# Optimization experiments

Measured on AMD Instinct MI355X. Metric: run time of the kernel, lower is better.

Reference implementation:

```python
import jax, jax.numpy as jnp
import numpy as np

B, LQ, LK = 4, 2048, 2048
DQ, DK, DO = 1024, 1024, 1024


def setup_inputs() -> dict:
    key = jax.random.key(0)
    ks = jax.random.split(key, 9)
    s = 0.02
    return {
        "query_input": jax.random.normal(ks[0], (B, LQ, DQ), jnp.float32),
        "key_input": jax.random.normal(ks[1], (B, LK, DK), jnp.float32),
        "value_input": jax.random.normal(ks[2], (B, LK, DK), jnp.float32),
        "Wq": jax.random.normal(ks[3], (DQ, DO), jnp.float32) * s,
        "bq": jax.random.normal(ks[4], (DO,), jnp.float32) * s,
        "Wk": jax.random.normal(ks[5], (DK, DO), jnp.float32) * s,
        "bk": jax.random.normal(ks[6], (DO,), jnp.float32) * s,
        "Wv": jax.random.normal(ks[7], (DK, DO), jnp.float32) * s,
        "bv": jax.random.normal(ks[8], (DO,), jnp.float32) * s,
    }


def reference(query_input, key_input, value_input, Wq, bq, Wk, bk, Wv, bv):
    scale = jnp.asarray(DO, query_input.dtype) ** 0.5
    q = query_input @ Wq + bq              # [B, Lq, D]
    k = key_input @ Wk + bk                # [B, Lk, D]
    v = value_input @ Wv + bv              # [B, Lk, D]
    attn = jnp.einsum("bqd,bkd->bqk", q, k) / scale
    attn = jax.nn.softmax(attn, axis=-1)
    return jnp.einsum("bqk,bkd->bqd", attn, v)
```

## Files before the change

### kernel.cpp

```cpp
#include <hip/hip_runtime.h>

typedef _Float16 f16x8 __attribute__((ext_vector_type(8)));
typedef _Float16 f16x4 __attribute__((ext_vector_type(4)));
typedef float f32x4 __attribute__((ext_vector_type(4)));
typedef int   v4i   __attribute__((ext_vector_type(4)));

__device__ __forceinline__ void lds_load16(const _Float16* g, _Float16* l) {
    __builtin_amdgcn_global_load_lds(
        (const __attribute__((address_space(1))) void*)g,
        (__attribute__((address_space(3))) void*)l,
        16, 0, 0);
}

__device__ __forceinline__ f16x8 ldsr(unsigned a) {
    v4i r;
    asm volatile("ds_read_b128 %0, %1" : "=v"(r) : "v"(a));
    return __builtin_bit_cast(f16x8, r);
}
template <int OFF>
__device__ __forceinline__ f16x8 ldsrO(unsigned a) {
    v4i r;
    if constexpr (OFF == 0)
        asm volatile("ds_read_b128 %0, %1" : "=v"(r) : "v"(a));
    else
        asm volatile("ds_read_b128 %0, %1 offset:%2" : "=v"(r) : "v"(a), "i"(OFF));
    return __builtin_bit_cast(f16x8, r);
}

__global__ __launch_bounds__(256, 3)
void gemm_proj(const _Float16* A0, const _Float16* B0, void* C0, const float* b0,
               const _Float16* A1, const _Float16* B1, void* C1, const float* b1,
               const _Float16* A2, const _Float16* B2, void* C2, const float* b2)
{
    constexpr int K = 1024, LDA = 1024, LDB = 1024, NT = K / 32;

    __shared__ __align__(16) _Float16 As[3][128 * 32];
    __shared__ __align__(16) _Float16 Bs[3][128 * 32];

    const int z  = blockIdx.z;
    const int bx = blockIdx.x, by = blockIdx.y;
    const int t    = threadIdx.x;
    const int w    = t >> 6;
    const int lane = t & 63;
    const int ln   = lane & 15;
    const int kq   = lane >> 4;
    const int wm   = (w & 1) * 64;
    const int wn   = (w >> 1) * 64;

    const _Float16* A = z == 0 ? A0 : z == 1 ? A1 : A2;
    const _Float16* B = z == 0 ? B0 : z == 1 ? B1 : B2;
    int m0, n0;
    if (z == 2) { m0 = (by & 7) * 128; n0 = (bx * 8 + (by >> 3)) * 128; }
    else        { m0 = (bx * 8 + (by >> 3)) * 128; n0 = (by & 7) * 128; }

    const int r4 = t >> 2;
    const int sc = ((t & 3) ^ ((t >> 3) & 3)) * 8;
    const _Float16* gA = A + (size_t)(m0 + r4) * LDA + sc;
    const _Float16* gB = B + (size_t)(n0 + r4) * LDB + sc;
    _Float16* const lA = &As[0][0] + w * 512;
    _Float16* const lB = &Bs[0][0] + w * 512;

    auto stage = [&](unsigned bufE, int kt) {
        lds_load16(gA + kt * 32,                     lA + bufE);
        lds_load16(gA + (size_t)64 * LDA + kt * 32,  lA + bufE + 2048);
        lds_load16(gB + kt * 32,                     lB + bufE);
        lds_load16(gB + (size_t)64 * LDB + kt * 32,  lB + bufE + 2048);
    };

    const int sk = (kq ^ ((ln >> 1) & 3)) * 16;
    const unsigned uA0 = (unsigned)(uintptr_t)(__attribute__((address_space(3))) _Float16*)&As[0][0];
    const unsigned uB0 = (unsigned)(uintptr_t)(__attribute__((address_space(3))) _Float16*)&Bs[0][0];
    const unsigned vAbase = uA0 + (wm + ln) * 64 + sk;
    const unsigned vBbase = uB0 + (wn + ln) * 64 + sk;

    f32x4 acc[4][4] = {};

    stage(0, 0);
    stage(4096, 1);
    asm volatile("s_waitcnt vmcnt(4)" ::: "memory");
    __builtin_amdgcn_s_barrier();
    __builtin_amdgcn_sched_barrier(0);

    unsigned offR = 0;
    unsigned offW = 8192;

    for (int kc = 0; kc < NT; ++kc) {
        const unsigned aA = vAbase + offR;
        const unsigned aB = vBbase + offR;
        f16x8 af[4], bf[4];
        af[0] = ldsrO<0>(aA);    af[1] = ldsrO<1024>(aA);
        af[2] = ldsrO<2048>(aA); af[3] = ldsrO<3072>(aA);
        bf[0] = ldsrO<0>(aB);    bf[1] = ldsrO<1024>(aB);
        bf[2] = ldsrO<2048>(aB); bf[3] = ldsrO<3072>(aB);

        const bool pf = (kc + 2 < NT);
        if (pf) stage(offW, kc + 2);

        asm volatile("s_waitcnt lgkmcnt(0)" ::: "memory");
        __builtin_amdgcn_sched_barrier(0);
        __builtin_amdgcn_s_setprio(1);
#pragma unroll
        for (int i = 0; i < 4; ++i)
#pragma unroll
            for (int j = 0; j < 4; ++j)
                acc[i][j] = __builtin_amdgcn_mfma_f32_16x16x32_f16(af[i], bf[j], acc[i][j], 0, 0, 0);
        __builtin_amdgcn_s_setprio(0);
        __builtin_amdgcn_sched_barrier(0);

        if (pf) asm volatile("s_waitcnt vmcnt(4)" ::: "memory");
        else    asm volatile("s_waitcnt vmcnt(0)" ::: "memory");
        __builtin_amdgcn_s_barrier();
        __builtin_amdgcn_sched_barrier(0);

        offR = (offR == 16384u) ? 0u : offR + 8192u;
        offW = (offW == 8192u)  ? 0u : offW + 4096u;
    }

    _Float16* Cp = (_Float16*)(z == 0 ? C0 : z == 1 ? C1 : C2);
    const float* bp = z == 0 ? b0 : z == 1 ? b1 : b2;
    const int ldc = (z == 2) ? 8192 : 1024;
#pragma unroll
    for (int i = 0; i < 4; ++i) {
        const int rbase = m0 + wm + i * 16 + kq * 4;
#pragma unroll
        for (int j = 0; j < 4; ++j) {
            const int gcol = n0 + wn + j * 16 + ln;
#pragma unroll
            for (int r = 0; r < 4; ++r) {
                float vv = acc[i][j][r] + (z == 2 ? bp[rbase + r] : bp[gcol]);
                Cp[(size_t)(rbase + r) * ldc + gcol] = (_Float16)vv;
            }
        }
    }
}

template <int MODE>
__global__ __launch_bounds__(512, 2)
void gemm_attn(const _Float16* A0, const _Float16* B0, void* C0, float* rowsum)
{
    constexpr int BM  = (MODE == 5) ? 128 : 256;
    constexpr int K   = (MODE == 5) ? 2048 : 1024;
    constexpr int LDA = (MODE == 5) ? 2048 : 1024;
    constexpr int LDB = (MODE == 5) ? 8192 : 1024;
    constexpr int NT  = K / 64;
    constexpr int MI  = BM / 32;
    constexpr int MH  = MI / 2;
    constexpr int LA  = BM / 64;

    __shared__ __align__(16) _Float16 As[2][BM * 64];
    __shared__ __align__(16) _Float16 Bs[2][256 * 64];

    const int bx = blockIdx.x, by = blockIdx.y;
    const int t    = threadIdx.x;
    const int w    = t >> 6;
    const int lane = t & 63;
    const int ln   = lane & 15;
    const int kq   = lane >> 4;
    const int wm   = (w >> 2) * (BM / 2);
    const int wn   = (w & 3) * 64;

    const _Float16* A;
    const _Float16* B;
    size_t cbase = 0;
    int m0, n0, z;

    if (MODE == 3) {
        z = blockIdx.z;
        A = A0 + (size_t)z * 2048 * 1024;
        B = B0 + (size_t)z * 2048 * 1024;
        cbase = (size_t)z * 2048 * 2048;
        rowsum += z * 2048;
        m0 = ((bx & 3) * 2 + (by >> 2)) * 256;
        n0 = ((bx >> 2) * 4 + (by & 3)) * 256;
    } else {
        z = (blockIdx.z << 1) | (bx >> 2);
        A = A0 + (size_t)z * 2048 * 2048;
        B = B0 + (size_t)z * 2048;
        cbase = (size_t)z * 2048 * 1024;
        rowsum += z * 2048;
        m0 = by * 128;
        n0 = (bx & 3) * 256;
    }

    const int r6 = t >> 3;
    const int cw = ((t & 7) ^ (r6 & 7)) * 8;
    const _Float16* gA = A + (size_t)(m0 + r6) * LDA + cw;
    const _Float16* gB = B + (size_t)(n0 + r6) * LDB + cw;

    auto stA = [&](int b, int kt, int s) {
        lds_load16(gA + (size_t)(s * 64) * LDA + kt * 64, As[b] + s * 4096 + w * 512);
    };
    auto stB = [&](int b, int kt, int s) {
        lds_load16(gB + (size_t)(s * 64) * LDB + kt * 64, Bs[b] + s * 4096 + w * 512);
    };

    const int xr  = ln & 7;
    const int sk0 = ((0 + kq) ^ xr) * 8;
    const int sk1 = ((4 + kq) ^ xr) * 8;
    const int ra  = (wm + ln) * 64;
    const int rb  = (wn + ln) * 64;

    const unsigned uA0 = (unsigned)(uintptr_t)(__attribute__((address_space(3))) _Float16*)&As[0][0];
    const unsigned uA1 = (unsigned)(uintptr_t)(__attribute__((address_space(3))) _Float16*)&As[1][0];
    const unsigned uB0 = (unsigned)(uintptr_t)(__attribute__((address_space(3))) _Float16*)&Bs[0][0];
    const unsigned uB1 = (unsigned)(uintptr_t)(__attribute__((address_space(3))) _Float16*)&Bs[1][0];
    const unsigned aA[2][2] = { { uA0 + 2u * (ra + sk0), uA0 + 2u * (ra + sk1) },
                                { uA1 + 2u * (ra + sk0), uA1 + 2u * (ra + sk1) } };
    const unsigned aB[2][2] = { { uB0 + 2u * (rb + sk0), uB0 + 2u * (rb + sk1) },
                                { uB1 + 2u * (rb + sk0), uB1 + 2u * (rb + sk1) } };

    f16x8 af[MH][2], bf[4][2];
    f32x4 acc[MI][4] = {};

    {
#pragma unroll
        for (int s = 0; s < LA; ++s) stA(0, 0, s);
#pragma unroll
        for (int s = 0; s < 4; ++s)  stB(0, 0, s);
#pragma unroll
        for (int s = 0; s < LA; ++s) stA(1, 1, s);
#pragma unroll
        for (int s = 0; s < 4; ++s)  stB(1, 1, s);
    }
    if constexpr (MODE == 5) asm volatile("s_waitcnt vmcnt(6)" ::: "memory");
    else                     asm volatile("s_waitcnt vmcnt(8)" ::: "memory");
    __builtin_amdgcn_s_barrier();
    __builtin_amdgcn_sched_barrier(0);

#pragma unroll 2
    for (int kc = 0; kc < NT; ++kc) {
        const int  b  = kc & 1;
        const bool pf = (kc + 2 < NT);

#pragma unroll
        for (int i = 0; i < MH; ++i) {
            af[i][0] = ldsr(aA[b][0] + i * 2048);
            af[i][1] = ldsr(aA[b][1] + i * 2048);
        }
#pragma unroll
        for (int j = 0; j < 2; ++j) {
            bf[j][0] = ldsr(aB[b][0] + j * 2048);
            bf[j][1] = ldsr(aB[b][1] + j * 2048);
        }
        __builtin_amdgcn_s_barrier();
        asm volatile("s_waitcnt lgkmcnt(0)" ::: "memory");
        __builtin_amdgcn_sched_barrier(0);
        __builtin_amdgcn_s_setprio(1);
#pragma unroll
        for (int kh = 0; kh < 2; ++kh)
#pragma unroll
            for (int i = 0; i < MH; ++i)
#pragma unroll
                for (int j = 0; j < 2; ++j)
                    acc[i][j] = __builtin_amdgcn_mfma_f32_16x16x32_f16(af[i][kh], bf[j][kh], acc[i][j], 0, 0, 0);
        __builtin_amdgcn_s_setprio(0);
        __builtin_amdgcn_s_barrier();
        __builtin_amdgcn_sched_barrier(0);

#pragma unroll
        for (int j = 2; j < 4; ++j) {
            bf[j][0] = ldsr(aB[b][0] + j * 2048);
            bf[j][1] = ldsr(aB[b][1] + j * 2048);
        }
        if constexpr (LA == 4) {
            if (pf) { stA(b, kc + 2, 0); stA(b, kc + 2, 2); }
        }
        __builtin_amdgcn_s_barrier();
        asm volatile("s_waitcnt lgkmcnt(0)" ::: "memory");
        __builtin_amdgcn_sched_barrier(0);
        __builtin_amdgcn_s_setprio(1);
#pragma unroll
        for (int kh = 0; kh < 2; ++kh)
#pragma unroll
            for (int i = 0; i < MH; ++i)
#pragma unroll
                for (int j = 2; j < 4; ++j)
                    acc[i][j] = __builtin_amdgcn_mfma_f32_16x16x32_f16(af[i][kh], bf[j][kh], acc[i][j], 0, 0, 0);
        __builtin_amdgcn_s_setprio(0);
        __builtin_amdgcn_s_barrier();
        __builtin_amdgcn_sched_barrier(0);

#pragma unroll
        for (int i = 0; i < MH; ++i) {
            af[i][0] = ldsr(aA[b][0] + (i + MH) * 2048);
            af[i][1] = ldsr(aA[b][1] + (i + MH) * 2048);
        }
        if (pf) { stB(b, kc + 2, 0); stB(b, kc + 2, 1); stB(b, kc + 2, 2); }
        __builtin_amdgcn_s_barrier();
        asm volatile("s_waitcnt lgkmcnt(0)" ::: "memory");
        __builtin_amdgcn_sched_barrier(0);
        __builtin_amdgcn_s_setprio(1);
#pragma unroll
        for (int kh = 0; kh < 2; ++kh)
#pragma unroll
            for (int i = 0; i < MH; ++i)
#pragma unroll
                for (int j = 0; j < 2; ++j)
                    acc[i + MH][j] = __builtin_amdgcn_mfma_f32_16x16x32_f16(af[i][kh], bf[j][kh], acc[i + MH][j], 0, 0, 0);
        __builtin_amdgcn_s_setprio(0);
        __builtin_amdgcn_s_barrier();
        __builtin_amdgcn_sched_barrier(0);

        if (pf) {
            stB(b, kc + 2, 3);
            if constexpr (LA == 4) { stA(b, kc + 2, 1); stA(b, kc + 2, 3); }
            else                   { stA(b, kc + 2, 0); stA(b, kc + 2, 1); }
            if constexpr (MODE == 5) asm volatile("s_waitcnt vmcnt(6)" ::: "memory");
            else                     asm volatile("s_waitcnt vmcnt(8)" ::: "memory");
        } else if (kc + 1 < NT) {
            asm volatile("s_waitcnt vmcnt(0)" ::: "memory");
        }
        __builtin_amdgcn_s_barrier();
        __builtin_amdgcn_sched_barrier(0);
        __builtin_amdgcn_s_setprio(1);
#pragma unroll
        for (int kh = 0; kh < 2; ++kh)
#pragma unroll
            for (int i = 0; i < MH; ++i)
#pragma unroll
                for (int j = 2; j < 4; ++j)
                    acc[i + MH][j] = __builtin_amdgcn_mfma_f32_16x16x32_f16(af[i][kh], bf[j][kh], acc[i + MH][j], 0, 0, 0);
        __builtin_amdgcn_s_setprio(0);
        __builtin_amdgcn_s_barrier();
        __builtin_amdgcn_sched_barrier(0);
    }

    if (MODE == 3) {
        _Float16* Ch = (_Float16*)C0;
#pragma unroll
        for (int i = 0; i < MI; ++i) {
            const int rbase = m0 + wm + i * 16 + kq * 4;
            float rs[4] = {0.f, 0.f, 0.f, 0.f};
#pragma unroll
            for (int j = 0; j < 4; ++j) {
                const int gcol = n0 + wn + j * 16 + ln;
#pragma unroll
                for (int r = 0; r < 4; ++r) {
                    float e = __expf(acc[i][j][r] * 0.03125f);
                    Ch[cbase + (size_t)(rbase + r) * 2048 + gcol] = (_Float16)e;
                    rs[r] += e;
                }
            }
#pragma unroll
            for (int r = 0; r < 4; ++r) {
                float s = rs[r];
                s += __shfl_xor(s, 1);
                s += __shfl_xor(s, 2);
                s += __shfl_xor(s, 4);
                s += __shfl_xor(s, 8);
                if (ln == 0) atomicAdd(&rowsum[rbase + r], s);
            }
        }
    } else {
        float* Cf = (float*)C0;
#pragma unroll
        for (int i = 0; i < MI; ++i) {
            const int rbase = m0 + wm + i * 16 + kq * 4;
            float inv[4];
#pragma unroll
            for (int r = 0; r < 4; ++r) inv[r] = 1.f / rowsum[rbase + r];
#pragma unroll
            for (int j = 0; j < 4; ++j) {
                const int gcol = n0 + wn + j * 16 + ln;
#pragma unroll
                for (int r = 0; r < 4; ++r)
                    Cf[cbase + (size_t)(rbase + r) * 1024 + gcol] = acc[i][j][r] * inv[r];
            }
        }
    }
}

__global__ __launch_bounds__(256)
void prep(const float4* __restrict__ x0, _Float16* __restrict__ y0,
          const float4* __restrict__ x1, _Float16* __restrict__ y1,
          const float4* __restrict__ x2, _Float16* __restrict__ y2,
          const float* __restrict__ W0, _Float16* __restrict__ T0,
          const float* __restrict__ W1, _Float16* __restrict__ T1,
          const float* __restrict__ W2, _Float16* __restrict__ T2,
          float* __restrict__ rowsum)
{
    if (blockIdx.y < 3) {
        const size_t i = (size_t)blockIdx.x * 256 + threadIdx.x;
        const float4* x = blockIdx.y == 0 ? x0 : blockIdx.y == 1 ? x1 : x2;
        _Float16*    yy = blockIdx.y == 0 ? y0 : blockIdx.y == 1 ? y1 : y2;
        float4 f = x[i];
        f16x4 o = { (_Float16)f.x, (_Float16)f.y, (_Float16)f.z, (_Float16)f.w };
        *(f16x4*)(yy + i * 4) = o;
        if (blockIdx.y == 0 && blockIdx.x < 32)
            rowsum[blockIdx.x * 256 + threadIdx.x] = 0.f;
        return;
    }
    if (blockIdx.x >= 3072) return;
    const int zz = blockIdx.x >> 10;
    const int tb = blockIdx.x & 1023;
    const float* W = zz == 0 ? W0 : zz == 1 ? W1 : W2;
    _Float16*   WT = zz == 0 ? T0 : zz == 1 ? T1 : T2;
    __shared__ float tile[32][33];
    const int bxs = (tb & 31) * 32;
    const int bys = (tb >> 5) * 32;
    const int tx = threadIdx.x & 31;
    const int ty = threadIdx.x >> 5;
#pragma unroll
    for (int i = ty; i < 32; i += 8)
        tile[i][tx] = W[(size_t)(bys + i) * 1024 + bxs + tx];
    __syncthreads();
#pragma unroll
    for (int i = ty; i < 32; i += 8)
        WT[(size_t)(bxs + i) * 1024 + bys + tx] = (_Float16)tile[tx][i];
}

extern "C" void kernel_launch(void* const* d_in, const int* in_sizes, int n_in,
                              void* d_out, int out_size, void* d_ws, size_t ws_size,
                              hipStream_t stream)
{
    const float* Xq = (const float*)d_in[0];
    const float* Xk = (const float*)d_in[1];
    const float* Xv = (const float*)d_in[2];
    const float* Wq = (const float*)d_in[3];
    const float* bq = (const float*)d_in[4];
    const float* Wk = (const float*)d_in[5];
    const float* bk = (const float*)d_in[6];
    const float* Wv = (const float*)d_in[7];
    const float* bv = (const float*)d_in[8];
    float* out = (float*)d_out;

    const size_t XN = (size_t)8192 * 1024;
    const size_t WN = (size_t)1024 * 1024;

    _Float16* ws  = (_Float16*)d_ws;
    _Float16* Xqh = ws;
    _Float16* Xkh = Xqh + XN;
    _Float16* Xvh = Xkh + XN;
    _Float16* WqT = Xvh + XN;
    _Float16* WkT = WqT + WN;
    _Float16* WvT = WkT + WN;
    _Float16* qh  = WvT + WN;
    _Float16* kh  = qh + XN;
    _Float16* vT  = kh + XN;
    _Float16* S   = vT + XN;
    float* rowsum = (float*)(S + (size_t)4 * 2048 * 2048);

    {
        dim3 g(8192, 4);
        prep<<<g, 256, 0, stream>>>((const float4*)Xq, Xqh,
                                    (const float4*)Xk, Xkh,
                                    (const float4*)Xv, Xvh,
                                    Wq, WqT, Wk, WkT, Wv, WvT, rowsum);
    }

    {
        dim3 g(8, 64, 3);
        gemm_proj<<<g, 256, 0, stream>>>(
            Xqh, WqT, qh, bq,
            Xkh, WkT, kh, bk,
            WvT, Xvh, vT, bv);
    }

    {
        dim3 g(8, 8, 4);
        gemm_attn<3><<<g, 512, 0, stream>>>(qh, kh, S, rowsum);
    }

    {
        dim3 g(8, 16, 2);
        gemm_attn<5><<<g, 512, 0, stream>>>(S, vT, out, rowsum);
    }
}
```

Baseline: 298.9 us.

## Deepen projection GEMM pipeline to 4 LDS stages with register double-buffering

Adds a fourth LDS buffer to the projection GEMM and prefetches three k-tiles ahead instead of two. The LDS fragment reads for the next k-tile are issued before the current MFMA block, with a partial lgkmcnt wait, so LDS latency overlaps with matrix math. The extra shared memory and fragment registers force launch bounds down from 3 to 2 blocks per CU, which lowers occupancy. A vmcnt(4) wait alongside the deeper prefetch may also order waits loosely.

```diff
diff --git a/kernel.cpp b/kernel.cpp
--- a/kernel.cpp
+++ b/kernel.cpp
@@ -27,15 +27,15 @@
     return __builtin_bit_cast(f16x8, r);
 }
 
-__global__ __launch_bounds__(256, 3)
+__global__ __launch_bounds__(256, 2)
 void gemm_proj(const _Float16* A0, const _Float16* B0, void* C0, const float* b0,
                const _Float16* A1, const _Float16* B1, void* C1, const float* b1,
                const _Float16* A2, const _Float16* B2, void* C2, const float* b2)
 {
     constexpr int K = 1024, LDA = 1024, LDB = 1024, NT = K / 32;
 
-    __shared__ __align__(16) _Float16 As[3][128 * 32];
-    __shared__ __align__(16) _Float16 Bs[3][128 * 32];
+    __shared__ __align__(16) _Float16 As[4][128 * 32];
+    __shared__ __align__(16) _Float16 Bs[4][128 * 32];
 
     const int z  = blockIdx.z;
     const int bx = blockIdx.x, by = blockIdx.y;
@@ -74,46 +74,57 @@
     const unsigned vBbase = uB0 + (wn + ln) * 64 + sk;
 
     f32x4 acc[4][4] = {};
+    f16x8 afA[4], bfA[4], afB[4], bfB[4];
 
     stage(0, 0);
     stage(4096, 1);
+    stage(8192, 2);
     asm volatile("s_waitcnt vmcnt(4)" ::: "memory");
     __builtin_amdgcn_s_barrier();
     __builtin_amdgcn_sched_barrier(0);
-
-    unsigned offR = 0;
-    unsigned offW = 8192;
-
-    for (int kc = 0; kc < NT; ++kc) {
-        const unsigned aA = vAbase + offR;
-        const unsigned aB = vBbase + offR;
-        f16x8 af[4], bf[4];
-        af[0] = ldsrO<0>(aA);    af[1] = ldsrO<1024>(aA);
-        af[2] = ldsrO<2048>(aA); af[3] = ldsrO<3072>(aA);
-        bf[0] = ldsrO<0>(aB);    bf[1] = ldsrO<1024>(aB);
-        bf[2] = ldsrO<2048>(aB); bf[3] = ldsrO<3072>(aB);
-
-        const bool pf = (kc + 2 < NT);
-        if (pf) stage(offW, kc + 2);
-
-        asm volatile("s_waitcnt lgkmcnt(0)" ::: "memory");
+    afA[0] = ldsrO<0>(vAbase);    afA[1] = ldsrO<1024>(vAbase);
+    afA[2] = ldsrO<2048>(vAbase); afA[3] = ldsrO<3072>(vAbase);
+    bfA[0] = ldsrO<0>(vBbase);    bfA[1] = ldsrO<1024>(vBbase);
+    bfA[2] = ldsrO<2048>(vBbase); bfA[3] = ldsrO<3072>(vBbase);
+
+    unsigned offRd = 8192;
+    unsigned offW  = 12288;
+
+    auto step = [&](int kc, f16x8 (&ma)[4], f16x8 (&mb)[4],
+                            f16x8 (&ra)[4], f16x8 (&rb)[4]) {
+        const bool doRd = (kc + 1 < NT);
+        const bool doSt = (kc + 3 < NT);
+        if (doRd) {
+            const unsigned aA = vAbase + offRd;
+            const unsigned aB = vBbase + offRd;
+            ra[0] = ldsrO<0>(aA);    ra[1] = ldsrO<1024>(aA);
+            ra[2] = ldsrO<2048>(aA); ra[3] = ldsrO<3072>(aA);
+            rb[0] = ldsrO<0>(aB);    rb[1] = ldsrO<1024>(aB);
+            rb[2] = ldsrO<2048>(aB); rb[3] = ldsrO<3072>(aB);
+        }
+        if (doSt) stage(offW, kc + 3);
+        if (doRd) asm volatile("s_waitcnt lgkmcnt(8)" ::: "memory");
+        else      asm volatile("s_waitcnt lgkmcnt(0)" ::: "memory");
         __builtin_amdgcn_sched_barrier(0);
         __builtin_amdgcn_s_setprio(1);
 #pragma unroll
         for (int i = 0; i < 4; ++i)
 #pragma unroll
             for (int j = 0; j < 4; ++j)
-                acc[i][j] = __builtin_amdgcn_mfma_f32_16x16x32_f16(af[i], bf[j], acc[i][j], 0, 0, 0);
+                acc[i][j] = __builtin_amdgcn_mfma_f32_16x16x32_f16(ma[i], mb[j], acc[i][j], 0, 0, 0);
         __builtin_amdgcn_s_setprio(0);
         __builtin_amdgcn_sched_barrier(0);
-
-        if (pf) asm volatile("s_waitcnt vmcnt(4)" ::: "memory");
-        else    asm volatile("s_waitcnt vmcnt(0)" ::: "memory");
-        __builtin_amdgcn_s_barrier();
-        __builtin_amdgcn_sched_barrier(0);
-
-        offR = (offR == 16384u) ? 0u : offR + 8192u;
-        offW = (offW == 8192u)  ? 0u : offW + 4096u;
+        if (doSt) asm volatile("s_waitcnt vmcnt(4)" ::: "memory");
+        else      asm volatile("s_waitcnt vmcnt(0)" ::: "memory");
+        __builtin_amdgcn_s_barrier();
+        __builtin_amdgcn_sched_barrier(0);
+        offRd = (offRd == 24576u) ? 0u : offRd + 8192u;
+        offW  = (offW  == 12288u) ? 0u : offW  + 4096u;
+    };
+
+    for (int kc = 0; kc < NT; kc += 2) {
+        step(kc,     afA, bfA, afB, bfB);
+        step(kc + 1, afB, bfB, afA, bfA);
     }
 
     _Float16* Cp = (_Float16*)(z == 0 ? C0 : z == 1 ? C1 : C2);
```

New measurement: 304.7 us. No clear change (+1.9%).
